# Kernel optimization log

Hardware: AMD Instinct MI355X
Metric: run time of the kernel (lower is better)

The kernel has to match this reference:

```python
import jax, jax.numpy as jnp
import numpy as np

SW, FB, EMB, H = 96, 64, 512, 3   # seg_width, freq_bandwidth, embedding_dim, num_heads
B, T = 4, 1024
F = SW * FB


def setup_inputs() -> dict:
    key = jax.random.key(0)
    ks = jax.random.split(key, 12)
    s = 0.02
    dh = SW // H
    return {
        "x": jax.random.normal(ks[0], (B, T, F), jnp.float32),
        "o_enc": jax.random.randint(ks[1], (B, T), 0, 2, jnp.int32),
        "r_enc": jax.random.normal(ks[2], (B, T, EMB), jnp.float32),
        "Wq": jax.random.normal(ks[3], (SW, SW), jnp.float32) * s,
        "bq": jnp.zeros((SW,), jnp.float32),
        "Wk": jax.random.normal(ks[4], (SW, SW), jnp.float32) * s,
        "bk": jnp.zeros((SW,), jnp.float32),
        "Wv": jax.random.normal(ks[5], (SW, SW), jnp.float32) * s,
        "bv": jnp.zeros((SW,), jnp.float32),
        "Er": jax.random.normal(ks[6], (FB, dh), jnp.float32) * s,   # relative pos embeddings, max_len = FB
        "W1": jax.random.normal(ks[7], (SW, 4 * SW), jnp.float32) * s,
        "b1": jnp.zeros((4 * SW,), jnp.float32),
        "W2": jax.random.normal(ks[8], (4 * SW, SW), jnp.float32) * s,
        "b2": jnp.zeros((SW,), jnp.float32),
        "We": jax.random.normal(ks[9], (F, EMB), jnp.float32) * s,
        "be": jnp.zeros((EMB,), jnp.float32),
    }


def _skew(qer):
    # qer: (N, h, L, L) -> Srel via Music-Transformer skewing
    padded = jnp.pad(qer, ((0, 0), (0, 0), (0, 0), (1, 0)))      # (N,h,L,L+1)
    n, h, l, l1 = padded.shape
    return padded.reshape(n, h, l1, l)[:, :, 1:, :]               # (N,h,L,L)


def _rel_attention(x, Wq, bq, Wk, bk, Wv, bv, Er):
    # x: (N, L, D); relative global self-attention with causal mask
    N, L, D = x.shape
    dh = D // H

    def heads(t):
        return t.reshape(N, L, H, dh).transpose(0, 2, 1, 3)       # (N,h,L,dh)

    q = heads(x @ Wq + bq)
    k = heads(x @ Wk + bk)
    v = heads(x @ Wv + bv)
    qer = jnp.einsum('nhld,md->nhlm', q, Er)                      # (N,h,L,L)
    srel = _skew(qer)
    scores = (jnp.einsum('nhld,nhmd->nhlm', q, k) + srel) / jnp.sqrt(jnp.asarray(dh, x.dtype))
    causal = jnp.triu(jnp.ones((L, L), bool), 1)
    scores = jnp.where(causal, jnp.finfo(scores.dtype).min, scores)
    attn = jax.nn.softmax(scores, axis=-1)
    out = jnp.einsum('nhlm,nhmd->nhld', attn, v)
    return out.transpose(0, 2, 1, 3).reshape(N, L, D)


def _segmentwise_mean(data, block_ids):
    # data: (B,T,E), block_ids: (B,T) contiguous non-decreasing segment ids in [0,T)
    Bn, Tn, En = data.shape
    seg_sum = jax.vmap(lambda d, i: jax.ops.segment_sum(d, i, num_segments=Tn))(data, block_ids)
    cnt = jax.vmap(lambda i: jax.ops.segment_sum(jnp.ones_like(i), i, num_segments=Tn))(block_ids)
    means = seg_sum / jnp.maximum(cnt, 1).astype(data.dtype)[..., None]
    is_start = jnp.concatenate(
        [jnp.ones((Bn, 1), bool), block_ids[:, 1:] != block_ids[:, :-1]], axis=1)
    gathered = jnp.take_along_axis(means, block_ids[..., None], axis=1)   # (B,T,E)
    # original writes each block's mean only at the block's first position, zeros elsewhere
    return jnp.where(is_start[..., None], gathered, jnp.zeros((), data.dtype))


def reference(x, o_enc, r_enc, Wq, bq, Wk, bk, Wv, bv, Er, W1, b1, W2, b2, We, be):
    Bn, Tn, Fn = x.shape
    xr = x.reshape(Bn * Tn, SW, FB).transpose(0, 2, 1)            # (B*T, FB, SW)
    emb = _rel_attention(xr, Wq, bq, Wk, bk, Wv, bv, Er)
    emb = jax.nn.relu(emb @ W1 + b1) @ W2 + b2                    # FFN: SW -> 4SW -> SW
    emb = emb.transpose(0, 2, 1).reshape(Bn, Tn, Fn)
    emb = emb @ We + be                                           # (B,T,EMB)
    # nn.LayerNorm(emb.shape): normalize over the WHOLE tensor, no affine, eps=1e-8
    mu = emb.mean()
    var = ((emb - mu) ** 2).mean()
    emb = (emb - mu) / jnp.sqrt(var + 1e-8)
    # _regionalize: block ids from cumsum of binary boundary indicators
    block_ids = jnp.cumsum(o_enc, axis=1)
    block_ids = block_ids - block_ids[:, :1]                      # matches 'if b[0]==1: b -= 1'
    block_means = _segmentwise_mean(emb, block_ids)
    return block_means + r_enc + emb
```

## Files before the change

kernel.cpp:

```cpp
#include <hip/hip_runtime.h>
#include <hip/hip_bf16.h>


typedef __attribute__((ext_vector_type(8))) short bf16x8;
typedef __attribute__((ext_vector_type(4))) float f32x4;

struct PtrTab { const void* p[16]; };

enum : int {
  O_WQT = 0,
  O_BQ  = 9984,
  O_WKT = 10080,
  O_BK  = 20064,
  O_WVT = 20160,
  O_BV  = 30144,
  O_ER  = 30240,
  O_W1T = 32288,
  O_B1  = 72224,
  O_W2C = 72608,
  O_B2  = 118688,
  O_WET = 118784
};

__device__ __forceinline__ float b2f(__hip_bfloat16 v) { return __bfloat162float(v); }
__device__ __forceinline__ __hip_bfloat16 f2b(float v) { return __float2bfloat16(v); }

__global__ __launch_bounds__(256) void prep_kernel(PtrTab tab,
                                                   __hip_bfloat16* __restrict__ Wc,
                                                   float* __restrict__ sums)
{
    __shared__ __hip_bfloat16 tile[64][65];
    const int bid = blockIdx.x, tid = threadIdx.x;
    const int kt = bid % 96, nt = bid / 96;
    const float* We = (const float*)tab.p[14];
    const int k0 = kt * 64, n0 = nt * 64;
    for (int e = tid; e < 4096; e += 256) {
        int kk = e >> 6, nn = e & 63;
        tile[nn][kk] = f2b(We[(size_t)(k0 + kk) * 512 + n0 + nn]);
    }
    __syncthreads();
    __hip_bfloat16* dstT = Wc + O_WET + ((size_t)nt * 96 + kt) * 4096;
    for (int e = tid; e < 4096; e += 256) dstT[e] = tile[e >> 6][e & 63];

    const int g = bid * 256 + tid;
    const int stride = gridDim.x * 256;
    const float* Wq = (const float*)tab.p[3];
    const float* bq = (const float*)tab.p[4];
    const float* Wk = (const float*)tab.p[5];
    const float* bk = (const float*)tab.p[6];
    const float* Wv = (const float*)tab.p[7];
    const float* bv = (const float*)tab.p[8];
    const float* Er = (const float*)tab.p[9];
    const float* W1 = (const float*)tab.p[10];
    const float* b1 = (const float*)tab.p[11];
    const float* W2 = (const float*)tab.p[12];
    const float* b2 = (const float*)tab.p[13];

    for (int t = 0; t < 3; ++t) {
        const float* W = (t == 0 ? Wq : t == 1 ? Wk : Wv);
        __hip_bfloat16* d = Wc + t * 10080;
        for (int i = g; i < 9984; i += stride) {
            int j = i / 104, c = i - j * 104;
            d[i] = (c < 96) ? f2b(W[c * 96 + j]) : f2b(0.0f);
        }
    }
    for (int i = g; i < 96; i += stride) {
        Wc[O_BQ + i] = f2b(bq[i]);
        Wc[O_BK + i] = f2b(bk[i]);
        Wc[O_BV + i] = f2b(bv[i]);
        Wc[O_B2 + i] = f2b(b2[i]);
    }
    for (int i = g; i < 2048; i += stride) Wc[O_ER + i] = f2b(Er[i]);
    for (int i = g; i < 39936; i += stride) {
        int j = i / 104, c = i - j * 104;
        Wc[O_W1T + i] = (c < 96) ? f2b(W1[c * 384 + j]) : f2b(0.0f);
    }
    for (int i = g; i < 384; i += stride) Wc[O_B1 + i] = f2b(b1[i]);
    for (int i = g; i < 46080; i += stride) {
        int kc = i / 3840, r = i - kc * 3840;
        int nn = r / 40, kk = r - nn * 40;
        Wc[O_W2C + i] = (kk < 32) ? f2b(W2[(kc * 32 + kk) * 96 + nn]) : f2b(0.0f);
    }
    if (g < 2) sums[g] = 0.f;
}

__global__ __launch_bounds__(256) void attn_ffn_kernel(
    const float* __restrict__ x, const __hip_bfloat16* __restrict__ Wc,
    __hip_bfloat16* __restrict__ M)
{
    const int n = blockIdx.x, tid = threadIdx.x;
    const int w = tid >> 6, lane = tid & 63, quad = lane >> 4, ln = lane & 15;

    __shared__ __align__(16) char smem[50432];
    __hip_bfloat16* xs  = (__hip_bfloat16*)(smem);
    __hip_bfloat16* wb  = (__hip_bfloat16*)(smem + 13312);
    __hip_bfloat16* PB  = (__hip_bfloat16*)(smem + 13312);
    __hip_bfloat16* kS  = (__hip_bfloat16*)(smem + 23296);
    __hip_bfloat16* vT  = (__hip_bfloat16*)(smem + 36608);
    __hip_bfloat16* hid = (__hip_bfloat16*)(smem + 23296);

    const f32x4 z4 = {0.f, 0.f, 0.f, 0.f};
    const int rowb = 16 * w + quad * 4;

    bf16x8 wf[9], wfn[9];
    #pragma unroll
    for (int i = 0; i < 9; ++i)
        wf[i] = *(const bf16x8*)(Wc + O_WQT + ((i % 3) * 16 + ln) * 104 + (i / 3) * 32 + quad * 8);

    {
        const float* xb = x + (size_t)n * 6144;
        const int sb = w * 24;
        for (int c = 0; c < 3; ++c) {
            float v[8];
            #pragma unroll
            for (int j = 0; j < 8; ++j) v[j] = xb[(sb + c * 8 + j) * 64 + lane];
            union { __hip_bfloat16 h[8]; bf16x8 v8; } pk;
            #pragma unroll
            for (int j = 0; j < 8; ++j) pk.h[j] = f2b(v[j]);
            *(bf16x8*)(xs + lane * 104 + sb + c * 8) = pk.v8;
        }
    }
    __syncthreads();

    bf16x8 aqr[3];

    for (int st = 0; st < 6; ++st) {
        const int t = st >> 1, half = st & 1;
        if (st < 5) {
            const __hip_bfloat16* nb = Wc + ((st + 1) >> 1) * 10080 + ((st + 1) & 1) * 4992;
            #pragma unroll
            for (int i = 0; i < 9; ++i)
                wfn[i] = *(const bf16x8*)(nb + ((i % 3) * 16 + ln) * 104 + (i / 3) * 32 + quad * 8);
        }
        f32x4 acc[3] = {z4, z4, z4};
        #pragma unroll
        for (int ks = 0; ks < 3; ++ks) {
            bf16x8 a = *(const bf16x8*)(xs + (16 * w + ln) * 104 + ks * 32 + quad * 8);
            #pragma unroll
            for (int ct = 0; ct < 3; ++ct)
                acc[ct] = __builtin_amdgcn_mfma_f32_16x16x32_bf16(a, wf[ks * 3 + ct], acc[ct], 0, 0, 0);
        }
        const int j0 = half * 48;
        const __hip_bfloat16* bt = Wc + 9984 + t * 10080;
        #pragma unroll
        for (int ct = 0; ct < 3; ++ct) {
            int col = j0 + ct * 16 + ln;
            float bb = b2f(bt[col]);
            if (t < 2) {
                #pragma unroll
                for (int r = 0; r < 4; ++r)
                    kS[(rowb + r) * 104 + col] = f2b(acc[ct][r] + bb);
            } else {
                union { __hip_bfloat16 h4[4]; uint2 u; } pk;
                #pragma unroll
                for (int r = 0; r < 4; ++r) pk.h4[r] = f2b(acc[ct][r] + bb);
                *(uint2*)(vT + col * 72 + rowb) = pk.u;
            }
        }
        if (t == 0 && half == 1) {
            #pragma unroll
            for (int h = 0; h < 3; ++h)
                aqr[h] = *(const bf16x8*)(kS + (16 * w + ln) * 104 + h * 32 + quad * 8);
        }
        #pragma unroll
        for (int i = 0; i < 9; ++i) wf[i] = wfn[i];
    }

    bf16x8 erf[4];
    #pragma unroll
    for (int tn = 0; tn < 4; ++tn)
        erf[tn] = *(const bf16x8*)(Wc + O_ER + (16 * tn + ln) * 32 + quad * 8);
    __syncthreads();

    bf16x8 pf0, pf1, pf2;
    {
        const bf16x8* src = (const bf16x8*)(Wc + O_W1T);
        pf0 = src[tid]; pf1 = src[tid + 256];
        if (tid + 512 < 624) pf2 = src[tid + 512];
    }

    for (int h = 0; h < 3; ++h) {
        const int c0 = h * 32;
        bf16x8 aq = aqr[h];
        #pragma unroll
        for (int tn = 0; tn < 4; ++tn) {
            f32x4 q4 = __builtin_amdgcn_mfma_f32_16x16x32_bf16(aq, erf[tn], z4, 0, 0, 0);
            #pragma unroll
            for (int r = 0; r < 4; ++r)
                PB[(rowb + r) * 72 + 16 * tn + ln] = f2b(q4[r]);
        }
        float sco[4][4];
        #pragma unroll
        for (int tn = 0; tn < 4; ++tn) {
            bf16x8 kf = *(const bf16x8*)(kS + (16 * tn + ln) * 104 + c0 + quad * 8);
            f32x4 s1 = __builtin_amdgcn_mfma_f32_16x16x32_bf16(aq, kf, z4, 0, 0, 0);
            #pragma unroll
            for (int r = 0; r < 4; ++r) sco[tn][r] = s1[r];
        }
        #pragma unroll
        for (int tn = 0; tn < 4; ++tn)
            #pragma unroll
            for (int r = 0; r < 4; ++r) {
                int row = rowb + r, col = 16 * tn + ln;
                if (col <= row)
                    sco[tn][r] = (sco[tn][r] + b2f(PB[row * 72 + col + 63 - row]))
                                 * 0.17677669529663687f;
                else
                    sco[tn][r] = -3.0e38f;
            }
        float mx[4], sm[4];
        #pragma unroll
        for (int r = 0; r < 4; ++r) {
            float m0 = fmaxf(fmaxf(sco[0][r], sco[1][r]), fmaxf(sco[2][r], sco[3][r]));
            #pragma unroll
            for (int d = 1; d < 16; d <<= 1) m0 = fmaxf(m0, __shfl_xor(m0, d, 64));
            mx[r] = m0;
        }
        #pragma unroll
        for (int tn = 0; tn < 4; ++tn)
            #pragma unroll
            for (int r = 0; r < 4; ++r) sco[tn][r] = __expf(sco[tn][r] - mx[r]);
        #pragma unroll
        for (int r = 0; r < 4; ++r) {
            float s0 = sco[0][r] + sco[1][r] + sco[2][r] + sco[3][r];
            #pragma unroll
            for (int d = 1; d < 16; d <<= 1) s0 += __shfl_xor(s0, d, 64);
            sm[r] = 1.0f / s0;
        }
        #pragma unroll
        for (int tn = 0; tn < 4; ++tn)
            #pragma unroll
            for (int r = 0; r < 4; ++r)
                PB[(rowb + r) * 72 + 16 * tn + ln] = f2b(sco[tn][r] * sm[r]);
        f32x4 oacc[2] = {z4, z4};
        #pragma unroll
        for (int ks2 = 0; ks2 < 2; ++ks2) {
            bf16x8 pa = *(const bf16x8*)(PB + (16 * w + ln) * 72 + ks2 * 32 + quad * 8);
            #pragma unroll
            for (int t2 = 0; t2 < 2; ++t2) {
                bf16x8 vb = *(const bf16x8*)(vT + (c0 + 16 * t2 + ln) * 72 + ks2 * 32 + quad * 8);
                oacc[t2] = __builtin_amdgcn_mfma_f32_16x16x32_bf16(pa, vb, oacc[t2], 0, 0, 0);
            }
        }
        #pragma unroll
        for (int t2 = 0; t2 < 2; ++t2)
            #pragma unroll
            for (int r = 0; r < 4; ++r)
                xs[(rowb + r) * 104 + c0 + 16 * t2 + ln] = f2b(oacc[t2][r]);
    }
    __syncthreads();

    f32x4 acc2[6] = {z4, z4, z4, z4, z4, z4};
    bf16x8 w2f[6], w2fn[6];
    for (int jh = 0; jh < 2; ++jh) {
        for (int cc = 0; cc < 4; ++cc) {
            const int j0g = jh * 192 + cc * 48;
            __syncthreads();
            {
                bf16x8* dst = (bf16x8*)wb;
                dst[tid] = pf0;
                dst[tid + 256] = pf1;
                if (tid + 512 < 624) dst[tid + 512] = pf2;
                if (cc < 3) {
                    const bf16x8* src = (const bf16x8*)(Wc + O_W1T + jh * 19968 + (cc + 1) * 4992);
                    pf0 = src[tid]; pf1 = src[tid + 256];
                    if (tid + 512 < 624) pf2 = src[tid + 512];
                } else {
                    const __hip_bfloat16* nb = Wc + O_W2C + (jh * 6) * 3840;
                    #pragma unroll
                    for (int ct = 0; ct < 6; ++ct)
                        w2f[ct] = *(const bf16x8*)(nb + (ct * 16 + ln) * 40 + quad * 8);
                }
            }
            __syncthreads();
            f32x4 a1[3] = {z4, z4, z4};
            #pragma unroll
            for (int ks = 0; ks < 3; ++ks) {
                bf16x8 a = *(const bf16x8*)(xs + (16 * w + ln) * 104 + ks * 32 + quad * 8);
                #pragma unroll
                for (int ct = 0; ct < 3; ++ct) {
                    bf16x8 b = *(const bf16x8*)(wb + (ct * 16 + ln) * 104 + ks * 32 + quad * 8);
                    a1[ct] = __builtin_amdgcn_mfma_f32_16x16x32_bf16(a, b, a1[ct], 0, 0, 0);
                }
            }
            #pragma unroll
            for (int ct = 0; ct < 3; ++ct) {
                int colg = j0g + ct * 16 + ln;
                int coll = cc * 48 + ct * 16 + ln;
                float bb = b2f(Wc[O_B1 + colg]);
                #pragma unroll
                for (int r = 0; r < 4; ++r)
                    hid[(rowb + r) * 200 + coll] = f2b(fmaxf(a1[ct][r] + bb, 0.f));
            }
        }
        for (int kc = 0; kc < 6; ++kc) {
            if (kc < 5) {
                const __hip_bfloat16* nb = Wc + O_W2C + (jh * 6 + kc + 1) * 3840;
                #pragma unroll
                for (int ct = 0; ct < 6; ++ct)
                    w2fn[ct] = *(const bf16x8*)(nb + (ct * 16 + ln) * 40 + quad * 8);
            } else if (jh == 0) {
                const bf16x8* src = (const bf16x8*)(Wc + O_W1T + 19968);
                pf0 = src[tid]; pf1 = src[tid + 256];
                if (tid + 512 < 624) pf2 = src[tid + 512];
            }
            bf16x8 a = *(const bf16x8*)(hid + (16 * w + ln) * 200 + kc * 32 + quad * 8);
            #pragma unroll
            for (int ct = 0; ct < 6; ++ct)
                acc2[ct] = __builtin_amdgcn_mfma_f32_16x16x32_bf16(a, w2f[ct], acc2[ct], 0, 0, 0);
            if (kc < 5) {
                #pragma unroll
                for (int ct = 0; ct < 6; ++ct) w2f[ct] = w2fn[ct];
            }
        }
    }

    __hip_bfloat16* Mg = M + (size_t)n * 6144;
    #pragma unroll
    for (int ct = 0; ct < 6; ++ct) {
        int d = ct * 16 + ln;
        float bb = b2f(Wc[O_B2 + d]);
        union { __hip_bfloat16 h4[4]; uint2 u; } pk;
        #pragma unroll
        for (int r = 0; r < 4; ++r) pk.h4[r] = f2b(acc2[ct][r] + bb);
        *(uint2*)((char*)Mg + (size_t)(d * 64 + rowb) * 2) = pk.u;
    }
}

__global__ __launch_bounds__(256) void gemm_kernel(
    const __hip_bfloat16* __restrict__ A,
    const __hip_bfloat16* __restrict__ Wc,
    const float* __restrict__ be,
    float* __restrict__ Y,
    float* __restrict__ sums)
{
    __shared__ __align__(16) __hip_bfloat16 As[2][64 * 72];
    __shared__ __align__(16) __hip_bfloat16 Bs[2][64 * 72];
    const int row0 = blockIdx.x * 64, nt = blockIdx.y, col0 = nt * 64;
    const int tid = threadIdx.x;
    const int w = tid >> 6, lane = tid & 63, quad = lane >> 4, ln = lane & 15;
    const int r0 = tid >> 3, c0_ = (tid & 7) * 8;
    const int r1 = r0 + 32,  c1_ = c0_;
    const size_t abase0 = (size_t)(row0 + r0) * 6144 + c0_;
    const size_t abase1 = (size_t)(row0 + r1) * 6144 + c1_;
    const __hip_bfloat16* Bsrc = Wc + O_WET + (size_t)nt * 96 * 4096;
    const size_t bbase0 = (size_t)r0 * 64 + c0_;
    const size_t bbase1 = (size_t)r1 * 64 + c1_;

    const f32x4 z4 = {0.f, 0.f, 0.f, 0.f};
    f32x4 acc[4] = {z4, z4, z4, z4};

    bf16x8 pa0 = *(const bf16x8*)(A + abase0);
    bf16x8 pa1 = *(const bf16x8*)(A + abase1);
    bf16x8 pb0 = *(const bf16x8*)(Bsrc + bbase0);
    bf16x8 pb1 = *(const bf16x8*)(Bsrc + bbase1);
    *(bf16x8*)(&As[0][r0 * 72 + c0_]) = pa0;
    *(bf16x8*)(&As[0][r1 * 72 + c1_]) = pa1;
    *(bf16x8*)(&Bs[0][r0 * 72 + c0_]) = pb0;
    *(bf16x8*)(&Bs[0][r1 * 72 + c1_]) = pb1;
    __syncthreads();

    for (int kt = 0; kt < 96; ++kt) {
        const int cur = kt & 1;
        if (kt < 95) {
            pa0 = *(const bf16x8*)(A + abase0 + (kt + 1) * 64);
            pa1 = *(const bf16x8*)(A + abase1 + (kt + 1) * 64);
            pb0 = *(const bf16x8*)(Bsrc + (size_t)(kt + 1) * 4096 + bbase0);
            pb1 = *(const bf16x8*)(Bsrc + (size_t)(kt + 1) * 4096 + bbase1);
        }
        #pragma unroll
        for (int ks = 0; ks < 2; ++ks) {
            bf16x8 a = *(const bf16x8*)(&As[cur][(16 * w + ln) * 72 + ks * 32 + quad * 8]);
            #pragma unroll
            for (int tn = 0; tn < 4; ++tn) {
                bf16x8 b = *(const bf16x8*)(&Bs[cur][(16 * tn + ln) * 72 + ks * 32 + quad * 8]);
                acc[tn] = __builtin_amdgcn_mfma_f32_16x16x32_bf16(a, b, acc[tn], 0, 0, 0);
            }
        }
        if (kt < 95) {
            *(bf16x8*)(&As[cur ^ 1][r0 * 72 + c0_]) = pa0;
            *(bf16x8*)(&As[cur ^ 1][r1 * 72 + c1_]) = pa1;
            *(bf16x8*)(&Bs[cur ^ 1][r0 * 72 + c0_]) = pb0;
            *(bf16x8*)(&Bs[cur ^ 1][r1 * 72 + c1_]) = pb1;
        }
        __syncthreads();
    }
    float s = 0.f, s2 = 0.f;
    #pragma unroll
    for (int tn = 0; tn < 4; ++tn) {
        int col = col0 + 16 * tn + ln;
        float bb = be[col];
        #pragma unroll
        for (int r = 0; r < 4; ++r) {
            float v = acc[tn][r] + bb;
            Y[(size_t)(row0 + 16 * w + quad * 4 + r) * 512 + col] = v;
            s += v; s2 += v * v;
        }
    }
    #pragma unroll
    for (int off = 1; off < 64; off <<= 1) {
        s  += __shfl_xor(s, off, 64);
        s2 += __shfl_xor(s2, off, 64);
    }
    __shared__ float r1s[4], r2s[4];
    if (lane == 0) { r1s[w] = s; r2s[w] = s2; }
    __syncthreads();
    if (tid == 0) {
        atomicAdd(&sums[0], r1s[0] + r1s[1] + r1s[2] + r1s[3]);
        atomicAdd(&sums[1], r2s[0] + r2s[1] + r2s[2] + r2s[3]);
    }
}

__global__ __launch_bounds__(256) void segid_kernel(const int* __restrict__ o_enc,
                                                    int* __restrict__ bids) {
    __shared__ int ts[256];
    const int b = blockIdx.x, tid = threadIdx.x;
    const int* o = o_enc + b * 1024;
    int v0 = o[4 * tid], v1 = o[4 * tid + 1], v2 = o[4 * tid + 2], v3 = o[4 * tid + 3];
    int p0 = v0, p1 = p0 + v1, p2 = p1 + v2, p3 = p2 + v3;
    ts[tid] = p3;
    __syncthreads();
    for (int off = 1; off < 256; off <<= 1) {
        int mine = ts[tid];
        int add = (tid >= off) ? ts[tid - off] : 0;
        __syncthreads();
        ts[tid] = mine + add;
        __syncthreads();
    }
    const int excl = (tid > 0) ? ts[tid - 1] : 0;
    const int off0 = o[0];
    int* bid = bids + b * 1024;
    bid[4 * tid]     = excl + p0 - off0;
    bid[4 * tid + 1] = excl + p1 - off0;
    bid[4 * tid + 2] = excl + p2 - off0;
    bid[4 * tid + 3] = excl + p3 - off0;
}

__global__ __launch_bounds__(256) void final_kernel(
    const float* __restrict__ Y, const int* __restrict__ bids,
    const float* __restrict__ sums, const float* __restrict__ r_enc,
    float* __restrict__ out)
{
    const int bt = blockIdx.x;
    const int b = bt >> 10, t = bt & 1023;
    const float mu = sums[0] * (1.0f / 2097152.0f);
    const float var = sums[1] * (1.0f / 2097152.0f) - mu * mu;
    const float rstd = rsqrtf(var + 1e-8f);
    const int* bid = bids + b * 1024;
    const int my = bid[t];
    const bool is_start = (t == 0) || (bid[t - 1] != my);
    int t2 = t + 1;
    float invc = 0.f;
    if (is_start) {
        while (t2 < 1024 && bid[t2] == my) ++t2;
        invc = 1.0f / (float)(t2 - t);
    }
    for (int e = threadIdx.x; e < 512; e += 256) {
        const size_t base = (size_t)bt * 512 + e;
        float res = (Y[base] - mu) * rstd + r_enc[base];
        if (is_start) {
            float s = 0.f;
            for (int tt = t; tt < t2; ++tt)
                s += (Y[((size_t)(b * 1024 + tt)) * 512 + e] - mu) * rstd;
            res += s * invc;
        }
        out[base] = res;
    }
}

extern "C" void kernel_launch(void* const* d_in, const int* in_sizes, int n_in,
                              void* d_out, int out_size, void* d_ws, size_t ws_size,
                              hipStream_t stream) {
    PtrTab tab;
    for (int i = 0; i < 16; ++i) tab.p[i] = d_in[i];

    char* ws = (char*)d_ws;
    __hip_bfloat16* M  = (__hip_bfloat16*)ws;
    float* Y           = (float*)(ws + 50331648);
    float* sums        = (float*)(ws + 58720256);
    int*   bids        = (int*)(ws + 58720320);
    __hip_bfloat16* Wc = (__hip_bfloat16*)(ws + 58736768);

    prep_kernel<<<768, 256, 0, stream>>>(tab, Wc, sums);
    attn_ffn_kernel<<<4096, 256, 0, stream>>>((const float*)d_in[0], Wc, M);
    gemm_kernel<<<dim3(64, 8), 256, 0, stream>>>(M, Wc, (const float*)d_in[15], Y, sums);
    segid_kernel<<<4, 256, 0, stream>>>((const int*)d_in[1], bids);
    final_kernel<<<4096, 256, 0, stream>>>(Y, bids, sums, (const float*)d_in[2], (float*)d_out);
}
```

Measured before the change: 394.3 us.

## Cut LDS and registers in attention/FFN kernel to raise occupancy

Shrinks shared memory from about 50KB to 40KB by removing the W1 staging buffer and reading W1/W2 fragments straight from global/L2, and sets launch_bounds(256,4) to target four blocks per CU. Drops the register double-buffered weight prefetch and instead keeps the x and attention-output A-fragments in registers. The attention step now computes transposed MFMAs so each lane owns one query row, writes the relative-position term already skewed into a scratch area, and reduces softmax with only two cross-lane shuffles. The cost is exposed global-load latency on weight reads, which higher occupancy is meant to hide.

Result: slower. 436.9 us (+10.8%).

```diff
diff --git a/kernel.cpp b/kernel.cpp
--- a/kernel.cpp
+++ b/kernel.cpp
@@ -84,28 +84,21 @@
     if (g < 2) sums[g] = 0.f;
 }
 
-__global__ __launch_bounds__(256) void attn_ffn_kernel(
+__global__ __launch_bounds__(256, 4) void attn_ffn_kernel(
     const float* __restrict__ x, const __hip_bfloat16* __restrict__ Wc,
     __hip_bfloat16* __restrict__ M)
 {
     const int n = blockIdx.x, tid = threadIdx.x;
     const int w = tid >> 6, lane = tid & 63, quad = lane >> 4, ln = lane & 15;
 
-    __shared__ __align__(16) char smem[50432];
+    __shared__ __align__(16) char smem[40448];
     __hip_bfloat16* xs  = (__hip_bfloat16*)(smem);
-    __hip_bfloat16* wb  = (__hip_bfloat16*)(smem + 13312);
-    __hip_bfloat16* PB  = (__hip_bfloat16*)(smem + 13312);
-    __hip_bfloat16* kS  = (__hip_bfloat16*)(smem + 23296);
-    __hip_bfloat16* vT  = (__hip_bfloat16*)(smem + 36608);
-    __hip_bfloat16* hid = (__hip_bfloat16*)(smem + 23296);
+    __hip_bfloat16* kS  = (__hip_bfloat16*)(smem + 13312);
+    __hip_bfloat16* vT  = (__hip_bfloat16*)(smem + 26624);
+    __hip_bfloat16* hid = (__hip_bfloat16*)(smem + 13312);
 
     const f32x4 z4 = {0.f, 0.f, 0.f, 0.f};
     const int rowb = 16 * w + quad * 4;
-
-    bf16x8 wf[9], wfn[9];
-    #pragma unroll
-    for (int i = 0; i < 9; ++i)
-        wf[i] = *(const bf16x8*)(Wc + O_WQT + ((i % 3) * 16 + ln) * 104 + (i / 3) * 32 + quad * 8);
 
     {
         const float* xb = x + (size_t)n * 6144;
@@ -122,24 +115,26 @@
     }
     __syncthreads();
 
+    bf16x8 af[3];
+    #pragma unroll
+    for (int ks = 0; ks < 3; ++ks)
+        af[ks] = *(const bf16x8*)(xs + (16 * w + ln) * 104 + ks * 32 + quad * 8);
+
     bf16x8 aqr[3];
 
     for (int st = 0; st < 6; ++st) {
         const int t = st >> 1, half = st & 1;
-        if (st < 5) {
-            const __hip_bfloat16* nb = Wc + ((st + 1) >> 1) * 10080 + ((st + 1) & 1) * 4992;
-            #pragma unroll
-            for (int i = 0; i < 9; ++i)
-                wfn[i] = *(const bf16x8*)(nb + ((i % 3) * 16 + ln) * 104 + (i / 3) * 32 + quad * 8);
-        }
+        const __hip_bfloat16* wsrc = Wc + t * 10080 + half * 4992;
+        bf16x8 wf[9];
+        #pragma unroll
+        for (int i = 0; i < 9; ++i)
+            wf[i] = *(const bf16x8*)(wsrc + ((i % 3) * 16 + ln) * 104 + (i / 3) * 32 + quad * 8);
         f32x4 acc[3] = {z4, z4, z4};
         #pragma unroll
-        for (int ks = 0; ks < 3; ++ks) {
-            bf16x8 a = *(const bf16x8*)(xs + (16 * w + ln) * 104 + ks * 32 + quad * 8);
+        for (int ks = 0; ks < 3; ++ks)
             #pragma unroll
             for (int ct = 0; ct < 3; ++ct)
-                acc[ct] = __builtin_amdgcn_mfma_f32_16x16x32_bf16(a, wf[ks * 3 + ct], acc[ct], 0, 0, 0);
-        }
+                acc[ct] = __builtin_amdgcn_mfma_f32_16x16x32_bf16(af[ks], wf[ks * 3 + ct], acc[ct], 0, 0, 0);
         const int j0 = half * 48;
         const __hip_bfloat16* bt = Wc + 9984 + t * 10080;
         #pragma unroll
@@ -162,8 +157,6 @@
             for (int h = 0; h < 3; ++h)
                 aqr[h] = *(const bf16x8*)(kS + (16 * w + ln) * 104 + h * 32 + quad * 8);
         }
-        #pragma unroll
-        for (int i = 0; i < 9; ++i) wf[i] = wfn[i];
     }
 
     bf16x8 erf[4];
@@ -172,120 +165,109 @@
         erf[tn] = *(const bf16x8*)(Wc + O_ER + (16 * tn + ln) * 32 + quad * 8);
     __syncthreads();
 
-    bf16x8 pf0, pf1, pf2;
-    {
-        const bf16x8* src = (const bf16x8*)(Wc + O_W1T);
-        pf0 = src[tid]; pf1 = src[tid + 256];
-        if (tid + 512 < 624) pf2 = src[tid + 512];
-    }
-
+    __hip_bfloat16* S2 = xs + 32;
+    const int ql = 16 * w + ln;
+    const int sshift = 63 - ql;
+    f32x4 oacc[3][2] = {{z4, z4}, {z4, z4}, {z4, z4}};
+
+    #pragma unroll
     for (int h = 0; h < 3; ++h) {
         const int c0 = h * 32;
         bf16x8 aq = aqr[h];
         #pragma unroll
         for (int tn = 0; tn < 4; ++tn) {
-            f32x4 q4 = __builtin_amdgcn_mfma_f32_16x16x32_bf16(aq, erf[tn], z4, 0, 0, 0);
-            #pragma unroll
-            for (int r = 0; r < 4; ++r)
-                PB[(rowb + r) * 72 + 16 * tn + ln] = f2b(q4[r]);
+            f32x4 q4 = __builtin_amdgcn_mfma_f32_16x16x32_bf16(erf[tn], aq, z4, 0, 0, 0);
+            #pragma unroll
+            for (int r = 0; r < 4; ++r) {
+                int e = 16 * tn + 4 * quad + r;
+                if (e >= sshift) S2[ql * 104 + (e - sshift)] = f2b(q4[r]);
+            }
         }
         float sco[4][4];
         #pragma unroll
         for (int tn = 0; tn < 4; ++tn) {
             bf16x8 kf = *(const bf16x8*)(kS + (16 * tn + ln) * 104 + c0 + quad * 8);
-            f32x4 s1 = __builtin_amdgcn_mfma_f32_16x16x32_bf16(aq, kf, z4, 0, 0, 0);
+            f32x4 s1 = __builtin_amdgcn_mfma_f32_16x16x32_bf16(kf, aq, z4, 0, 0, 0);
             #pragma unroll
             for (int r = 0; r < 4; ++r) sco[tn][r] = s1[r];
         }
         #pragma unroll
+        for (int tn = 0; tn < 4; ++tn) {
+            union { __hip_bfloat16 h4[4]; uint2 u; } sr;
+            sr.u = *(const uint2*)(S2 + ql * 104 + 16 * tn + 4 * quad);
+            #pragma unroll
+            for (int r = 0; r < 4; ++r) {
+                int m = 16 * tn + 4 * quad + r;
+                sco[tn][r] = (m <= ql)
+                    ? (sco[tn][r] + b2f(sr.h4[r])) * 0.17677669529663687f
+                    : -3.0e38f;
+            }
+        }
+        float mt[4];
+        #pragma unroll
         for (int tn = 0; tn < 4; ++tn)
-            #pragma unroll
-            for (int r = 0; r < 4; ++r) {
-                int row = rowb + r, col = 16 * tn + ln;
-                if (col <= row)
-                    sco[tn][r] = (sco[tn][r] + b2f(PB[row * 72 + col + 63 - row]))
-                                 * 0.17677669529663687f;
-                else
-                    sco[tn][r] = -3.0e38f;
-            }
-        float mx[4], sm[4];
-        #pragma unroll
-        for (int r = 0; r < 4; ++r) {
-            float m0 = fmaxf(fmaxf(sco[0][r], sco[1][r]), fmaxf(sco[2][r], sco[3][r]));
-            #pragma unroll
-            for (int d = 1; d < 16; d <<= 1) m0 = fmaxf(m0, __shfl_xor(m0, d, 64));
-            mx[r] = m0;
-        }
-        #pragma unroll
-        for (int tn = 0; tn < 4; ++tn)
-            #pragma unroll
-            for (int r = 0; r < 4; ++r) sco[tn][r] = __expf(sco[tn][r] - mx[r]);
-        #pragma unroll
-        for (int r = 0; r < 4; ++r) {
-            float s0 = sco[0][r] + sco[1][r] + sco[2][r] + sco[3][r];
-            #pragma unroll
-            for (int d = 1; d < 16; d <<= 1) s0 += __shfl_xor(s0, d, 64);
-            sm[r] = 1.0f / s0;
-        }
-        #pragma unroll
-        for (int tn = 0; tn < 4; ++tn)
-            #pragma unroll
-            for (int r = 0; r < 4; ++r)
-                PB[(rowb + r) * 72 + 16 * tn + ln] = f2b(sco[tn][r] * sm[r]);
-        f32x4 oacc[2] = {z4, z4};
+            mt[tn] = fmaxf(fmaxf(sco[tn][0], sco[tn][1]), fmaxf(sco[tn][2], sco[tn][3]));
+        float mx = fmaxf(fmaxf(mt[0], mt[1]), fmaxf(mt[2], mt[3]));
+        mx = fmaxf(mx, __shfl_xor(mx, 16, 64));
+        mx = fmaxf(mx, __shfl_xor(mx, 32, 64));
+        float st_[4];
+        #pragma unroll
+        for (int tn = 0; tn < 4; ++tn) {
+            #pragma unroll
+            for (int r = 0; r < 4; ++r) sco[tn][r] = __expf(sco[tn][r] - mx);
+            st_[tn] = (sco[tn][0] + sco[tn][1]) + (sco[tn][2] + sco[tn][3]);
+        }
+        float sum = (st_[0] + st_[1]) + (st_[2] + st_[3]);
+        sum += __shfl_xor(sum, 16, 64);
+        sum += __shfl_xor(sum, 32, 64);
+        const float inv = 1.0f / sum;
+        #pragma unroll
+        for (int tn = 0; tn < 4; ++tn) {
+            union { __hip_bfloat16 h4[4]; uint2 u; } pk;
+            #pragma unroll
+            for (int r = 0; r < 4; ++r) pk.h4[r] = f2b(sco[tn][r] * inv);
+            *(uint2*)(S2 + ql * 104 + 16 * tn + 4 * quad) = pk.u;
+        }
         #pragma unroll
         for (int ks2 = 0; ks2 < 2; ++ks2) {
-            bf16x8 pa = *(const bf16x8*)(PB + (16 * w + ln) * 72 + ks2 * 32 + quad * 8);
+            bf16x8 pa = *(const bf16x8*)(S2 + ql * 104 + ks2 * 32 + quad * 8);
             #pragma unroll
             for (int t2 = 0; t2 < 2; ++t2) {
                 bf16x8 vb = *(const bf16x8*)(vT + (c0 + 16 * t2 + ln) * 72 + ks2 * 32 + quad * 8);
-                oacc[t2] = __builtin_amdgcn_mfma_f32_16x16x32_bf16(pa, vb, oacc[t2], 0, 0, 0);
-            }
-        }
+                oacc[h][t2] = __builtin_amdgcn_mfma_f32_16x16x32_bf16(pa, vb, oacc[h][t2], 0, 0, 0);
+            }
+        }
+    }
+    #pragma unroll
+    for (int h = 0; h < 3; ++h)
         #pragma unroll
         for (int t2 = 0; t2 < 2; ++t2)
             #pragma unroll
             for (int r = 0; r < 4; ++r)
-                xs[(rowb + r) * 104 + c0 + 16 * t2 + ln] = f2b(oacc[t2][r]);
-    }
-    __syncthreads();
+                xs[(rowb + r) * 104 + h * 32 + 16 * t2 + ln] = f2b(oacc[h][t2][r]);
+    __syncthreads();
+
+    bf16x8 cf[3];
+    #pragma unroll
+    for (int ks = 0; ks < 3; ++ks)
+        cf[ks] = *(const bf16x8*)(xs + (16 * w + ln) * 104 + ks * 32 + quad * 8);
 
     f32x4 acc2[6] = {z4, z4, z4, z4, z4, z4};
-    bf16x8 w2f[6], w2fn[6];
     for (int jh = 0; jh < 2; ++jh) {
+        #pragma unroll
         for (int cc = 0; cc < 4; ++cc) {
-            const int j0g = jh * 192 + cc * 48;
-            __syncthreads();
-            {
-                bf16x8* dst = (bf16x8*)wb;
-                dst[tid] = pf0;
-                dst[tid + 256] = pf1;
-                if (tid + 512 < 624) dst[tid + 512] = pf2;
-                if (cc < 3) {
-                    const bf16x8* src = (const bf16x8*)(Wc + O_W1T + jh * 19968 + (cc + 1) * 4992);
-                    pf0 = src[tid]; pf1 = src[tid + 256];
-                    if (tid + 512 < 624) pf2 = src[tid + 512];
-                } else {
-                    const __hip_bfloat16* nb = Wc + O_W2C + (jh * 6) * 3840;
-                    #pragma unroll
-                    for (int ct = 0; ct < 6; ++ct)
-                        w2f[ct] = *(const bf16x8*)(nb + (ct * 16 + ln) * 40 + quad * 8);
-                }
-            }
-            __syncthreads();
+            const __hip_bfloat16* wsrc = Wc + O_W1T + (size_t)(jh * 192 + cc * 48) * 104;
             f32x4 a1[3] = {z4, z4, z4};
             #pragma unroll
-            for (int ks = 0; ks < 3; ++ks) {
-                bf16x8 a = *(const bf16x8*)(xs + (16 * w + ln) * 104 + ks * 32 + quad * 8);
+            for (int ks = 0; ks < 3; ++ks)
                 #pragma unroll
                 for (int ct = 0; ct < 3; ++ct) {
-                    bf16x8 b = *(const bf16x8*)(wb + (ct * 16 + ln) * 104 + ks * 32 + quad * 8);
-                    a1[ct] = __builtin_amdgcn_mfma_f32_16x16x32_bf16(a, b, a1[ct], 0, 0, 0);
+                    bf16x8 b = *(const bf16x8*)(wsrc + (ct * 16 + ln) * 104 + ks * 32 + quad * 8);
+                    a1[ct] = __builtin_amdgcn_mfma_f32_16x16x32_bf16(cf[ks], b, a1[ct], 0, 0, 0);
                 }
-            }
             #pragma unroll
             for (int ct = 0; ct < 3; ++ct) {
-                int colg = j0g + ct * 16 + ln;
+                int colg = jh * 192 + cc * 48 + ct * 16 + ln;
                 int coll = cc * 48 + ct * 16 + ln;
                 float bb = b2f(Wc[O_B1 + colg]);
                 #pragma unroll
@@ -293,24 +275,14 @@
                     hid[(rowb + r) * 200 + coll] = f2b(fmaxf(a1[ct][r] + bb, 0.f));
             }
         }
+        #pragma unroll
         for (int kc = 0; kc < 6; ++kc) {
-            if (kc < 5) {
-                const __hip_bfloat16* nb = Wc + O_W2C + (jh * 6 + kc + 1) * 3840;
-                #pragma unroll
-                for (int ct = 0; ct < 6; ++ct)
-                    w2fn[ct] = *(const bf16x8*)(nb + (ct * 16 + ln) * 40 + quad * 8);
-            } else if (jh == 0) {
-                const bf16x8* src = (const bf16x8*)(Wc + O_W1T + 19968);
-                pf0 = src[tid]; pf1 = src[tid + 256];
-                if (tid + 512 < 624) pf2 = src[tid + 512];
-            }
+            const __hip_bfloat16* nb = Wc + O_W2C + (size_t)(jh * 6 + kc) * 3840;
             bf16x8 a = *(const bf16x8*)(hid + (16 * w + ln) * 200 + kc * 32 + quad * 8);
             #pragma unroll
-            for (int ct = 0; ct < 6; ++ct)
-                acc2[ct] = __builtin_amdgcn_mfma_f32_16x16x32_bf16(a, w2f[ct], acc2[ct], 0, 0, 0);
-            if (kc < 5) {
-                #pragma unroll
-                for (int ct = 0; ct < 6; ++ct) w2f[ct] = w2fn[ct];
+            for (int ct = 0; ct < 6; ++ct) {
+                bf16x8 wfr = *(const bf16x8*)(nb + (ct * 16 + ln) * 40 + quad * 8);
+                acc2[ct] = __builtin_amdgcn_mfma_f32_16x16x32_bf16(a, wfr, acc2[ct], 0, 0, 0);
             }
         }
     }
```
